# Kernel tuning notes

Measured on AMD Instinct MI355X. Metric: run time of the kernel, lower is better.

Reference implementation:

```python
import jax, jax.numpy as jnp
from jax import lax
import numpy as np

HOP = 256          # hop_length
WIN = 1024         # window_size = 4 * hop
PAD = (WIN - HOP) // 2
B, T = 16, 262144
P = 22             # LPC order (number of denominator coeffs, excluding leading 1)


def hann_periodic(n):
    # torch.hann_window default (periodic=True)
    return 0.5 * (1.0 - jnp.cos(2.0 * jnp.pi * jnp.arange(n, dtype=jnp.float32) / n))


def setup_inputs() -> dict:
    key = jax.random.key(0)
    k1, k2, k3 = jax.random.split(key, 3)
    F = T // HOP
    ex = jax.random.normal(k1, (B, T), jnp.float32)
    gain = jax.random.uniform(k2, (B, F), jnp.float32, minval=0.1, maxval=1.0)
    # scale so sum_k |a_k| < 1 -> stable IIR (avoids overflow in the recursion)
    a = jax.random.normal(k3, (B, F, P), jnp.float32) * 0.01
    return {"ex": ex, "gain": gain, "a": a}


def lpc_synthesis(x, gain, a):
    # x: [N, W], gain: [N], a: [N, P]
    # all-pole IIR: y[n] = gain * x[n] - sum_{k=1..P} a[k-1] * y[n-k]
    Pn = a.shape[-1]

    def step(carry, xt):
        # carry: [N, P] past outputs, most recent first; xt: [N]
        y = gain * xt - jnp.einsum('np,np->n', a, carry)
        carry = jnp.concatenate([y[:, None], carry[:, :-1]], axis=1)
        return carry, y

    init = jnp.zeros((x.shape[0], Pn), x.dtype)
    _, ys = lax.scan(step, init, x.T)  # ys: [W, N]
    return ys.T


def overlap_add(frames, hop, out_len):
    # frames: [B, F, W]; scatter-add frame f at offset f*hop
    Bn, Fn, Wn = frames.shape
    idx = (jnp.arange(Fn)[:, None] * hop + jnp.arange(Wn)[None, :]).reshape(-1)
    out = jnp.zeros((Bn, out_len), frames.dtype)
    return out.at[:, idx].add(frames.reshape(Bn, -1))


def reference(ex, gain, a):
    Bn, Tn = ex.shape
    Fn = Tn // HOP  # number of frames after unfold
    w = hann_periodic(WIN)

    # pad + unfold -> [B, F, W]
    exp = jnp.pad(ex, ((0, 0), (PAD, PAD)))
    fidx = jnp.arange(Fn)[:, None] * HOP + jnp.arange(WIN)[None, :]
    unfolded = exp[:, fidx]

    # per-frame recursive LPC synthesis filter
    filt = lpc_synthesis(
        unfolded.reshape(-1, WIN), gain.reshape(-1), a.reshape(-1, P)
    ).reshape(Bn, Fn, WIN)

    # windowed overlap-add (equivalent to conv_transpose1d with diag(window) kernel)
    L = (Fn - 1) * HOP + WIN
    y = overlap_add(filt * w, HOP, L)[:, PAD:PAD + Tn]
    norm = overlap_add(jnp.broadcast_to(w, (1, Fn, WIN)), HOP, L)[0, PAD:PAD + Tn]
    return y / norm
```

## Files before the change

### kernel.cpp

```cpp
#include <hip/hip_runtime.h>

namespace {

typedef float v2f __attribute__((ext_vector_type(2)));

constexpr int T_LEN = 262144;
constexpr int NF    = 1024;

__device__ __forceinline__ float qsum(float x) {
    x += __int_as_float(__builtin_amdgcn_update_dpp(
             0, __float_as_int(x), 0xB1, 0xF, 0xF, true));
    x += __int_as_float(__builtin_amdgcn_update_dpp(
             0, __float_as_int(x), 0x4E, 0xF, 0xF, true));
    return x;
}

template <bool CK>
__device__ __forceinline__ void ld4(const float* __restrict__ exb, int xi,
                                    float4 (&buf)[4]) {
    #pragma unroll
    for (int q = 0; q < 4; ++q) {
        const int idx = xi + q * 4;
        if (CK) {
            float4 v = make_float4(0.f, 0.f, 0.f, 0.f);
            if (idx >= 0) v = *(const float4*)(exb + idx);
            buf[q] = v;
        } else {
            buf[q] = *(const float4*)(exb + idx);
        }
    }
}

__device__ __forceinline__ void iir4(const float4& x4, v2f (&sv)[11],
                                     const v2f (&mav)[11], float gv,
                                     float (&yo)[4]) {
    const float xv[4] = {x4.x, x4.y, x4.z, x4.w};
    #pragma unroll
    for (int u = 0; u < 4; ++u) {
        float y   = fmaf(gv, xv[u], sv[0].x);
        float s11 = sv[0].y;
        v2f yy = (v2f){y, y};
        #pragma unroll
        for (int j = 0; j < 10; ++j)
            sv[j] = __builtin_elementwise_fma(mav[j], yy, sv[j + 1]);
        sv[10].x = fmaf(mav[10].x, y, s11);
        sv[10].y = mav[10].y * y;
        yo[u] = y;
    }
}

__device__ __forceinline__ void proc16w(const float4 (&buf)[4], v2f (&sv)[11],
                                        const v2f (&mav)[11], float gv) {
    float yd[4];
    #pragma unroll
    for (int q = 0; q < 4; ++q) iir4(buf[q], sv, mav, gv, yd);
}

template <bool EDGE>
__device__ __forceinline__ void proc16o(const float4 (&buf)[4], v2f (&sv)[11],
                                        const v2f (&mav)[11], float gv,
                                        float& rev, float cA, float cB,
                                        bool st, float* __restrict__ outp) {
    #pragma unroll
    for (int q = 0; q < 4; ++q) {
        float y[4];
        iir4(buf[q], sv, mav, gv, y);
        float o[4];
        #pragma unroll
        for (int u = 0; u < 4; ++u) {
            float c = __builtin_amdgcn_cosf(rev);
            rev += (1.0f / 1024.0f);
            float wl = fmaf(cA, c, cB);
            float v  = wl * y[u];
            if (EDGE) {
                o[u] = qsum(v) * __builtin_amdgcn_rcpf(qsum(wl));
            } else {
                o[u] = qsum(v);
            }
        }
        if (st) *(float4*)(outp + q * 4) = make_float4(o[0], o[1], o[2], o[3]);
    }
}

__global__ __launch_bounds__(64, 2)
void lpc_ola_kernel(const float* __restrict__ ex,
                    const float* __restrict__ gain,
                    const float* __restrict__ a,
                    float* __restrict__ out)
{
    const int lane = threadIdx.x;
    const int w    = blockIdx.x;
    const int wloc = w & 127;
    const bool chk  = (wloc == 0);
    const bool edge = (wloc == 0) | (wloc == 127);

    const int kk = lane & 3;
    const int jl = lane >> 2;
    const int tau = w * 16 + jl;
    const int b  = tau >> 11;
    const int i  = (tau & 2047) + 3;
    const int fi = i >> 1;
    const int f  = fi - kk;
    const bool fv = (unsigned)f < (unsigned)NF;
    const int fc = fv ? f : 0;
    const float mval = fv ? 1.f : 0.f;
    const float gv   = fv ? gain[b * NF + fc] : 0.f;

    v2f mav[11];
    {
        const float2* ap = (const float2*)(a + (size_t)(b * NF + fc) * 22);
        float man[22];
        #pragma unroll
        for (int j = 0; j < 11; ++j) {
            float2 t = ap[j];
            man[2 * j] = -t.x; man[2 * j + 1] = -t.y;
        }
        #pragma unroll
        for (int j = 0; j < 11; ++j) mav[j] = (v2f){man[j], man[j + 11]};
    }
    v2f sv[11];
    #pragma unroll
    for (int j = 0; j < 11; ++j) sv[j] = (v2f){0.f, 0.f};

    const float* exb = ex + (size_t)b * T_LEN;
    int xi = i * 128 - 512;
    const int m0k = kk * 256 + ((i & 1) << 7);
    float rev = (float)m0k * (1.0f / 1024.0f);
    const float scale = edge ? 0.5f : 0.25f;
    const float cA = -scale * mval, cB = scale * mval;
    float* outp0 = out + (size_t)b * T_LEN + (i * 128 - 384);

    float4 A[4], B[4];
    if (chk) { ld4<true >(exb, xi, A); xi += 16; ld4<true >(exb, xi, B); xi += 16; }
    else     { ld4<false>(exb, xi, A); xi += 16; ld4<false>(exb, xi, B); xi += 16; }

    #pragma unroll 1
    for (int it = 0; it < 4; ++it) {
        proc16w(A, sv, mav, gv);
        if (chk) ld4<true>(exb, xi, A); else ld4<false>(exb, xi, A);
        xi += 16;
        proc16w(B, sv, mav, gv);
        if (chk) ld4<true>(exb, xi, B); else ld4<false>(exb, xi, B);
        xi += 16;
    }

    if (!edge) {
        #pragma unroll 1
        for (int it = 0; it < 4; ++it) {
            const int sb = 2 * it;
            proc16o<false>(A, sv, mav, gv, rev, cA, cB,
                           kk == (sb >> 1), outp0 + sb * 16);
            if (it < 3) { ld4<false>(exb, xi, A); xi += 16; }
            proc16o<false>(B, sv, mav, gv, rev, cA, cB,
                           kk == ((sb + 1) >> 1), outp0 + (sb + 1) * 16);
            if (it < 3) { ld4<false>(exb, xi, B); xi += 16; }
        }
    } else {
        #pragma unroll 1
        for (int it = 0; it < 4; ++it) {
            const int sb = 2 * it;
            proc16o<true>(A, sv, mav, gv, rev, cA, cB,
                          kk == (sb >> 1), outp0 + sb * 16);
            if (it < 3) { ld4<false>(exb, xi, A); xi += 16; }
            proc16o<true>(B, sv, mav, gv, rev, cA, cB,
                          kk == ((sb + 1) >> 1), outp0 + (sb + 1) * 16);
            if (it < 3) { ld4<false>(exb, xi, B); xi += 16; }
        }
    }
}

}

extern "C" void kernel_launch(void* const* d_in, const int* in_sizes, int n_in,
                              void* d_out, int out_size, void* d_ws, size_t ws_size,
                              hipStream_t stream)
{
    (void)in_sizes; (void)n_in; (void)out_size; (void)d_ws; (void)ws_size;
    const float* ex   = (const float*)d_in[0];
    const float* gain = (const float*)d_in[1];
    const float* a    = (const float*)d_in[2];
    float* out        = (float*)d_out;

    dim3 grid(2048);
    dim3 block(64);
    hipLaunchKernelGGL(lpc_ola_kernel, grid, block, 0, stream, ex, gain, a, out);
}
```

Measured before the change: 89.55 us.

## Stage input samples, coefficients and outputs through LDS with coalesced block copies

Each block now cooperatively loads its padded input window and its per-frame LPC coefficients and gains into shared memory using coalesced float4 loads. The IIR recursion reads from LDS instead of issuing strided per-lane global loads, and outputs are written to LDS and then stored coalesced. This targets the uncoalesced, redundant global traffic of the previous per-lane loading scheme. The cost is extra LDS use, which may limit occupancy, and LDS latency inside the serial recursion. With a single 64-thread wave per block, the compiler-only fence relies on wave-synchronous behaviour rather than a real barrier.

```diff
diff --git a/kernel.cpp b/kernel.cpp
--- a/kernel.cpp
+++ b/kernel.cpp
@@ -6,6 +6,9 @@
 
 constexpr int T_LEN = 262144;
 constexpr int NF    = 1024;
+constexpr float INV1024 = 1.0f / 1024.0f;
+
+#define LDS_FENCE() asm volatile("" ::: "memory")
 
 __device__ __forceinline__ float qsum(float x) {
     x += __int_as_float(__builtin_amdgcn_update_dpp(
@@ -13,22 +16,6 @@
     x += __int_as_float(__builtin_amdgcn_update_dpp(
              0, __float_as_int(x), 0x4E, 0xF, 0xF, true));
     return x;
-}
-
-template <bool CK>
-__device__ __forceinline__ void ld4(const float* __restrict__ exb, int xi,
-                                    float4 (&buf)[4]) {
-    #pragma unroll
-    for (int q = 0; q < 4; ++q) {
-        const int idx = xi + q * 4;
-        if (CK) {
-            float4 v = make_float4(0.f, 0.f, 0.f, 0.f);
-            if (idx >= 0) v = *(const float4*)(exb + idx);
-            buf[q] = v;
-        } else {
-            buf[q] = *(const float4*)(exb + idx);
-        }
-    }
 }
 
 __device__ __forceinline__ void iir4(const float4& x4, v2f (&sv)[11],
@@ -49,36 +36,32 @@
     }
 }
 
-__device__ __forceinline__ void proc16w(const float4 (&buf)[4], v2f (&sv)[11],
-                                        const v2f (&mav)[11], float gv) {
-    float yd[4];
-    #pragma unroll
-    for (int q = 0; q < 4; ++q) iir4(buf[q], sv, mav, gv, yd);
-}
-
 template <bool EDGE>
-__device__ __forceinline__ void proc16o(const float4 (&buf)[4], v2f (&sv)[11],
-                                        const v2f (&mav)[11], float gv,
-                                        float& rev, float cA, float cB,
-                                        bool st, float* __restrict__ outp) {
-    #pragma unroll
-    for (int q = 0; q < 4; ++q) {
-        float y[4];
-        iir4(buf[q], sv, mav, gv, y);
-        float o[4];
+__device__ __forceinline__ void outphase(const float* __restrict__ exo,
+                                         float* __restrict__ oto,
+                                         v2f (&sv)[11], const v2f (&mav)[11],
+                                         float gv, float rev, float cA, float cB,
+                                         int kk) {
+    #pragma unroll 1
+    for (int sb = 0; sb < 8; ++sb) {
+        const bool st = (kk == (sb >> 1));
         #pragma unroll
-        for (int u = 0; u < 4; ++u) {
-            float c = __builtin_amdgcn_cosf(rev);
-            rev += (1.0f / 1024.0f);
-            float wl = fmaf(cA, c, cB);
-            float v  = wl * y[u];
-            if (EDGE) {
-                o[u] = qsum(v) * __builtin_amdgcn_rcpf(qsum(wl));
-            } else {
-                o[u] = qsum(v);
+        for (int qg = 0; qg < 4; ++qg) {
+            float4 x4 = *(const float4*)(exo + sb * 16 + qg * 4);
+            float y[4];
+            iir4(x4, sv, mav, gv, y);
+            float o[4];
+            #pragma unroll
+            for (int u = 0; u < 4; ++u) {
+                float c = __builtin_amdgcn_cosf(rev);
+                rev += INV1024;
+                float wl = fmaf(cA, c, cB);
+                if (EDGE) o[u] = qsum(wl * y[u]) * __builtin_amdgcn_rcpf(qsum(wl));
+                else      o[u] = qsum(wl * y[u]);
             }
+            if (st) *(float4*)(oto + sb * 16 + qg * 4) =
+                        make_float4(o[0], o[1], o[2], o[3]);
         }
-        if (st) *(float4*)(outp + q * 4) = make_float4(o[0], o[1], o[2], o[3]);
     }
 }
 
@@ -88,31 +71,66 @@
                     const float* __restrict__ a,
                     float* __restrict__ out)
 {
+    __shared__ __align__(16) float exs[2240];
+    __shared__ __align__(16) float outs[2108];
+    __shared__ __align__(16) float cfs[288];
+
     const int lane = threadIdx.x;
     const int w    = blockIdx.x;
     const int wloc = w & 127;
-    const bool chk  = (wloc == 0);
+    const int b    = w >> 7;
     const bool edge = (wloc == 0) | (wloc == 127);
+
+    const int i0    = wloc * 16 + 3;
+    const int xbase = i0 * 128 - 512;
+    const int obase = i0 * 128 - 384;
+    const float* exb  = ex  + (size_t)b * T_LEN;
+    float*       outb = out + (size_t)b * T_LEN;
+
+    #pragma unroll
+    for (int r = 0; r < 9; ++r) {
+        const int idx = r * 256 + lane * 4;
+        if (idx < 2176) {
+            const int g = xbase + idx;
+            float4 v = make_float4(0.f, 0.f, 0.f, 0.f);
+            if ((unsigned)g < (unsigned)T_LEN) v = *(const float4*)(exb + g);
+            *(float4*)&exs[idx + ((idx >> 7) << 2)] = v;
+        }
+    }
+    const int fbase = wloc * 8 - 2;
+    #pragma unroll
+    for (int r = 0; r < 5; ++r) {
+        const int idx = r * 64 + lane;
+        if (idx < 288) {
+            const int q = (idx * 2731) >> 16;
+            const int c = idx - q * 24;
+            const int f = fbase + q;
+            float vv = 0.f;
+            if ((unsigned)f < (unsigned)NF) {
+                if (c < 22)       vv = a[(size_t)(b * NF + f) * 22 + c];
+                else if (c == 22) vv = gain[b * NF + f];
+            }
+            cfs[idx] = vv;
+        }
+    }
+    LDS_FENCE();
 
     const int kk = lane & 3;
     const int jl = lane >> 2;
-    const int tau = w * 16 + jl;
-    const int b  = tau >> 11;
-    const int i  = (tau & 2047) + 3;
+    const int i  = i0 + jl;
     const int fi = i >> 1;
     const int f  = fi - kk;
-    const bool fv = (unsigned)f < (unsigned)NF;
-    const int fc = fv ? f : 0;
-    const float mval = fv ? 1.f : 0.f;
-    const float gv   = fv ? gain[b * NF + fc] : 0.f;
+    const float mval = ((unsigned)f < (unsigned)NF) ? 1.f : 0.f;
+    const int q  = ((jl + 1) >> 1) + 3 - kk;
+    const float* cf = cfs + q * 24;
+    const float gv = cf[22];
 
     v2f mav[11];
     {
-        const float2* ap = (const float2*)(a + (size_t)(b * NF + fc) * 22);
         float man[22];
         #pragma unroll
         for (int j = 0; j < 11; ++j) {
-            float2 t = ap[j];
+            float2 t = ((const float2*)cf)[j];
             man[2 * j] = -t.x; man[2 * j + 1] = -t.y;
         }
         #pragma unroll
@@ -122,50 +140,36 @@
     #pragma unroll
     for (int j = 0; j < 11; ++j) sv[j] = (v2f){0.f, 0.f};
 
-    const float* exb = ex + (size_t)b * T_LEN;
-    int xi = i * 128 - 512;
-    const int m0k = kk * 256 + ((i & 1) << 7);
-    float rev = (float)m0k * (1.0f / 1024.0f);
+    const int e   = i & 1;
+    const int m0k = kk * 256 + (e << 7);
+    const float rev = (float)m0k * INV1024;
     const float scale = edge ? 0.5f : 0.25f;
     const float cA = -scale * mval, cB = scale * mval;
-    float* outp0 = out + (size_t)b * T_LEN + (i * 128 - 384);
 
-    float4 A[4], B[4];
-    if (chk) { ld4<true >(exb, xi, A); xi += 16; ld4<true >(exb, xi, B); xi += 16; }
-    else     { ld4<false>(exb, xi, A); xi += 16; ld4<false>(exb, xi, B); xi += 16; }
-
-    #pragma unroll 1
-    for (int it = 0; it < 4; ++it) {
-        proc16w(A, sv, mav, gv);
-        if (chk) ld4<true>(exb, xi, A); else ld4<false>(exb, xi, A);
-        xi += 16;
-        proc16w(B, sv, mav, gv);
-        if (chk) ld4<true>(exb, xi, B); else ld4<false>(exb, xi, B);
-        xi += 16;
+    const float* exw = exs + jl * 132;
+    {
+        float yd[4];
+        float4 Xa = *(const float4*)(exw);
+        #pragma unroll 1
+        for (int g = 0; g < 16; ++g) {
+            float4 Xb = *(const float4*)(exw + g * 8 + 4);
+            iir4(Xa, sv, mav, gv, yd);
+            if (g < 15) Xa = *(const float4*)(exw + g * 8 + 8);
+            iir4(Xb, sv, mav, gv, yd);
+        }
     }
 
-    if (!edge) {
-        #pragma unroll 1
-        for (int it = 0; it < 4; ++it) {
-            const int sb = 2 * it;
-            proc16o<false>(A, sv, mav, gv, rev, cA, cB,
-                           kk == (sb >> 1), outp0 + sb * 16);
-            if (it < 3) { ld4<false>(exb, xi, A); xi += 16; }
-            proc16o<false>(B, sv, mav, gv, rev, cA, cB,
-                           kk == ((sb + 1) >> 1), outp0 + (sb + 1) * 16);
-            if (it < 3) { ld4<false>(exb, xi, B); xi += 16; }
-        }
-    } else {
-        #pragma unroll 1
-        for (int it = 0; it < 4; ++it) {
-            const int sb = 2 * it;
-            proc16o<true>(A, sv, mav, gv, rev, cA, cB,
-                          kk == (sb >> 1), outp0 + sb * 16);
-            if (it < 3) { ld4<false>(exb, xi, A); xi += 16; }
-            proc16o<true>(B, sv, mav, gv, rev, cA, cB,
-                          kk == ((sb + 1) >> 1), outp0 + (sb + 1) * 16);
-            if (it < 3) { ld4<false>(exb, xi, B); xi += 16; }
-        }
+    const float* exo = exs + jl * 132 + 132;
+    float* oto = outs + jl * 132;
+    if (!edge) outphase<false>(exo, oto, sv, mav, gv, rev, cA, cB, kk);
+    else       outphase<true >(exo, oto, sv, mav, gv, rev, cA, cB, kk);
+
+    LDS_FENCE();
+    #pragma unroll
+    for (int r = 0; r < 8; ++r) {
+        const int gi = r * 256 + lane * 4;
+        float4 v = *(const float4*)&outs[gi + ((gi >> 7) << 2)];
+        *(float4*)(outb + obase + gi) = v;
     }
 }
 
```

New measurement: 94.63 us. 5.7% more time.
